# Optimization experiments

Hardware: AMD Instinct MI355X
Metric: run time of the kernel (lower is better)

Reference implementation:

```python
import jax, jax.numpy as jnp
import numpy as np

B, T, D, H = 2, 2048, 1024, 16  # batch, seq, hidden, heads; head_dim = 64


def setup_inputs() -> dict:
    key = jax.random.key(0)
    k1, k2, k3 = jax.random.split(key, 3)
    X = jax.random.normal(k1, (B, T, D), dtype=jnp.float32)
    # Dense(3*hidden_dim, use_bias=False): kernel [D, 3D]
    Wqkv = jax.random.normal(k2, (D, 3 * D), dtype=jnp.float32) / np.float32(np.sqrt(D))
    # Dense(hidden_dim, use_bias=False): kernel [D, D]
    Wproj = jax.random.normal(k3, (D, D), dtype=jnp.float32) / np.float32(np.sqrt(D))
    return {"X": X, "Wqkv": Wqkv, "Wproj": Wproj, "train": 0}


def reference(X, Wqkv, Wproj, train):
    # train=0 -> dropout is identity; the chunked online-softmax in the
    # original is mathematically exact softmax causal attention.
    b, t, d = X.shape
    hd = d // H
    qkv = X @ Wqkv                      # [B,T,3D]
    q, k, v = jnp.split(qkv, 3, axis=-1)
    q = q.reshape(b, t, H, hd)
    k = k.reshape(b, t, H, hd)
    v = v.reshape(b, t, H, hd)
    scale = 1.0 / jnp.sqrt(jnp.asarray(hd, dtype=X.dtype))
    scores = jnp.einsum('bqhd,bkhd->bhqk', q * scale, k)  # [B,H,T,T]
    causal = jnp.tril(jnp.ones((t, t), dtype=bool))
    scores = jnp.where(causal[None, None, :, :], scores, -jnp.inf)
    attn = jax.nn.softmax(scores, axis=-1)
    out = jnp.einsum('bhqk,bkhd->bqhd', attn, v).reshape(b, t, d)
    return out @ Wproj
```

## Files before the change

### kernel.cpp

```cpp
#include <hip/hip_runtime.h>


using u16 = unsigned short;
using u32 = unsigned int;

typedef __bf16 bf16x8 __attribute__((ext_vector_type(8)));
typedef __bf16 bf16x2 __attribute__((ext_vector_type(2)));
typedef float f32x4 __attribute__((ext_vector_type(4)));

#define DEV __device__ __forceinline__

DEV u16 f2bf(float f) { __bf16 h = (__bf16)f; return *(u16*)&h; }

DEV float bf2f(u16 v) {
  union { u32 u; float f; } x; x.u = (u32)v << 16; return x.f;
}

DEV u32 pk2(float lo, float hi) {
  bf16x2 t = {(__bf16)lo, (__bf16)hi};
  return *(u32*)&t;
}

DEV f32x4 mfma16(bf16x8 a, bf16x8 b, f32x4 c) {
  return __builtin_amdgcn_mfma_f32_16x16x32_bf16(a, b, c, 0, 0, 0);
}

DEV void gload_lds16(const void* g, void* l) {
  __builtin_amdgcn_global_load_lds(
      (const __attribute__((address_space(1))) void*)g,
      (__attribute__((address_space(3))) void*)l, 16, 0, 0);
}

DEV bf16x8 ld16(const u16* p) { return *(const bf16x8*)p; }

DEV void BAR() {
  __builtin_amdgcn_s_barrier();
  __builtin_amdgcn_sched_barrier(0);
}

DEV int vperm(int slot) {
  return ((((slot >> 4) & 2) | ((slot >> 2) & 1)) << 4) + (((slot >> 3) & 3) << 2) + (slot & 3);
}
DEV int vperm_inv(int k) {
  return (k & 0x23) | ((k & 0x10) >> 2) | ((k & 0x0c) << 1);
}


__global__ __launch_bounds__(256) void prep_kernel(
    const float* __restrict__ X, u16* __restrict__ Xb,
    const float* __restrict__ Wqkv, u16* __restrict__ Wqkvt,
    const float* __restrict__ Wproj, u16* __restrict__ Wprojt) {
  const int bid = blockIdx.x;
  const int t = threadIdx.x;

  if (bid < 2048) {
    int i = (bid * 256 + t) * 8;
    float4 a = *(const float4*)&X[i];
    float4 b = *(const float4*)&X[i + 4];
    union { u16 u[8]; uint4 v; } o;
    o.u[0] = f2bf(a.x); o.u[1] = f2bf(a.y); o.u[2] = f2bf(a.z); o.u[3] = f2bf(a.w);
    o.u[4] = f2bf(b.x); o.u[5] = f2bf(b.y); o.u[6] = f2bf(b.z); o.u[7] = f2bf(b.w);
    *(uint4*)&Xb[i] = o.v;
    return;
  }

  __shared__ float tile[64][65];
  const float* W; u16* Wt; int C, tb;
  if (bid < 2816) { W = Wqkv;  Wt = Wqkvt;  C = 3072; tb = bid - 2048; }
  else            { W = Wproj; Wt = Wprojt; C = 1024; tb = bid - 2816; }
  const int tilesC = C >> 6;
  const int tr = tb / tilesC, tc = tb % tilesC;
#pragma unroll
  for (int j = 0; j < 16; ++j) {
    int idx = j * 256 + t;
    int r = idx >> 6, c = idx & 63;
    tile[r][c] = W[(tr * 64 + r) * C + tc * 64 + c];
  }
  __syncthreads();
#pragma unroll
  for (int j = 0; j < 16; ++j) {
    int idx = j * 256 + t;
    int r = idx >> 6, c = idx & 63;
    Wt[(tc * 64 + r) * 1024 + tr * 64 + c] = f2bf(tile[c][r]);
  }
}


__global__ __launch_bounds__(512, 2) void gemm256_qkv_kernel(
    const u16* __restrict__ A, const u16* __restrict__ Bt,
    u16* __restrict__ Qb, u16* __restrict__ Kb, u16* __restrict__ VtP) {
  int bid = blockIdx.x;
  int bid2 = (bid & 7) * 24 + (bid >> 3);
  const int mt = bid2 / 12, nt = bid2 % 12;
  const int m0 = mt * 256, n0 = nt * 256;
  const int tid = threadIdx.x;
  const int wid = tid >> 6, lane = tid & 63;
  const int g = lane >> 4, li = lane & 15;
  const int wm = wid >> 2, wn = wid & 3;

  __shared__ __align__(16) u16 lds[65536];

  const int srow = lane >> 3;
  const int scol = ((lane & 7) * 8) ^ ((srow & 7) << 3);

  auto ISSUE = [&](int s, int kt) {
    const int p = kt & 1;
    const u16* base = (s < 2) ? &A[(size_t)(m0 + s * 128) * 1024]
                              : &Bt[(size_t)(n0 + (s - 2) * 128) * 1024];
#pragma unroll
    for (int is2 = 0; is2 < 2; ++is2) {
      int row = is2 * 64 + wid * 8 + srow;
      gload_lds16(&base[(size_t)row * 1024 + kt * 64 + scol],
                  &lds[s * 16384 + p * 8192 + is2 * 4096 + wid * 512]);
    }
  };

  auto LDA = [&](int p, int ks, bf16x8* aF) {
#pragma unroll
    for (int mi = 0; mi < 8; ++mi) {
      int row = mi * 16 + li;
      aF[mi] = ld16(&lds[wm * 16384 + p * 8192 + row * 64 +
                         ((ks * 32 + g * 8) ^ ((li & 7) << 3))]);
    }
  };
  auto LDB = [&](int p, int ks, bf16x8* bF) {
    int s = 2 + (wn >> 1);
#pragma unroll
    for (int ni = 0; ni < 4; ++ni) {
      int row = (wn & 1) * 64 + ni * 16 + li;
      bF[ni] = ld16(&lds[s * 16384 + p * 8192 + row * 64 +
                         ((ks * 32 + g * 8) ^ ((li & 7) << 3))]);
    }
  };

  f32x4 acc[8][4] = {};
  bf16x8 a0[8], a1[8], bF[4];

  ISSUE(0, 0); ISSUE(1, 0); ISSUE(2, 0); ISSUE(3, 0);
  ISSUE(0, 1); ISSUE(1, 1); ISSUE(2, 1);
  asm volatile("s_waitcnt vmcnt(6)" ::: "memory");
  BAR();

  for (int t = 0; t < 16; ++t) {
    const int p = t & 1;
    LDB(p, 0, bF);
    LDA(p, 0, a0);
    if (t + 1 < 16) ISSUE(3, t + 1);
    BAR();
    __builtin_amdgcn_s_setprio(1);
#pragma unroll
    for (int mi = 0; mi < 8; ++mi) {
      acc[mi][0] = mfma16(a0[mi], bF[0], acc[mi][0]);
      acc[mi][1] = mfma16(a0[mi], bF[1], acc[mi][1]);
    }
    __builtin_amdgcn_s_setprio(0);
    BAR();
    LDA(p, 1, a1);
    BAR();
    __builtin_amdgcn_s_setprio(1);
#pragma unroll
    for (int mi = 0; mi < 8; ++mi) {
      acc[mi][2] = mfma16(a0[mi], bF[2], acc[mi][2]);
      acc[mi][3] = mfma16(a0[mi], bF[3], acc[mi][3]);
    }
    __builtin_amdgcn_s_setprio(0);
    BAR();
    LDB(p, 1, bF);
    BAR();
    __builtin_amdgcn_s_setprio(1);
#pragma unroll
    for (int mi = 0; mi < 8; ++mi) {
      acc[mi][0] = mfma16(a1[mi], bF[0], acc[mi][0]);
      acc[mi][1] = mfma16(a1[mi], bF[1], acc[mi][1]);
    }
    __builtin_amdgcn_s_setprio(0);
    BAR();
    if (t + 2 < 16) { ISSUE(0, t + 2); ISSUE(1, t + 2); ISSUE(2, t + 2); }
    BAR();
    __builtin_amdgcn_s_setprio(1);
#pragma unroll
    for (int mi = 0; mi < 8; ++mi) {
      acc[mi][2] = mfma16(a1[mi], bF[2], acc[mi][2]);
      acc[mi][3] = mfma16(a1[mi], bF[3], acc[mi][3]);
    }
    __builtin_amdgcn_s_setprio(0);
    if (t + 2 < 16) {
      asm volatile("s_waitcnt vmcnt(6)" ::: "memory");
    } else {
      asm volatile("s_waitcnt vmcnt(0)" ::: "memory");
    }
    BAR();
  }

#pragma unroll
  for (int mi = 0; mi < 8; ++mi)
#pragma unroll
    for (int ni = 0; ni < 4; ++ni) {
      int cc = n0 + wn * 64 + ni * 16 + li;
      int which = cc >> 10, rem = cc & 1023;
      int h = rem >> 6, dd = rem & 63;
      int rbase = m0 + wm * 128 + mi * 16 + g * 4;
      int bb = rbase >> 11, tt = rbase & 2047;
      if (which == 2) {
        int slot0 = (tt & ~63) + vperm_inv(tt & 63);
        size_t di = ((size_t)(bb * 16 + h) * 64 + dd) * 2048 + slot0;
        uint2 wv;
        wv.x = pk2(acc[mi][ni][0], acc[mi][ni][1]);
        wv.y = pk2(acc[mi][ni][2], acc[mi][ni][3]);
        *(uint2*)&VtP[di] = wv;
      } else {
        u16* dst = which == 0 ? Qb : Kb;
        float sc = which == 0 ? 0.18033688f : 1.0f;
        size_t di = ((size_t)(bb * 16 + h) * 2048 + tt) * 64 + dd;
#pragma unroll
        for (int r = 0; r < 4; ++r) dst[di + (size_t)r * 64] = f2bf(acc[mi][ni][r] * sc);
      }
    }
}

__global__ __launch_bounds__(256) void gemm_proj_kernel(
    const u16* __restrict__ A, const u16* __restrict__ Bt, float* __restrict__ OF) {
  constexpr int NTN = 1024 / 128;
  const int mt = blockIdx.x / NTN, nt = blockIdx.x % NTN;
  const int m0 = mt * 128, n0 = nt * 128;
  const int tid = threadIdx.x;
  const int wid = tid >> 6, lane = tid & 63;
  const int g = lane >> 4, li = lane & 15;
  const int wm = wid >> 1, wn = wid & 1;

  __shared__ __align__(16) u16 As[2][128 * 64];
  __shared__ __align__(16) u16 Bs[2][128 * 64];

  f32x4 acc[4][4] = {};

  auto ISSUE = [&](int buf, int kt) {
#pragma unroll
    for (int iss = 0; iss < 4; ++iss) {
      int e = iss * 2048 + wid * 512 + lane * 8;
      int row = e >> 6;
      int kk = (e & 63) ^ ((row & 7) << 3);
      gload_lds16(&A[(size_t)(m0 + row) * 1024 + kt * 64 + kk], &As[buf][iss * 2048 + wid * 512]);
      gload_lds16(&Bt[(size_t)(n0 + row) * 1024 + kt * 64 + kk], &Bs[buf][iss * 2048 + wid * 512]);
    }
  };

  ISSUE(0, 0);
  __syncthreads();
  int cur = 0;

  for (int kt = 0; kt < 16; ++kt) {
    if (kt + 1 < 16) ISSUE(cur ^ 1, kt + 1);
#pragma unroll
    for (int ks = 0; ks < 2; ++ks) {
      bf16x8 af[4], bfr[4];
#pragma unroll
      for (int mi = 0; mi < 4; ++mi)
        af[mi] = ld16(&As[cur][(wm * 64 + mi * 16 + li) * 64 +
                               ((ks * 32 + g * 8) ^ ((li & 7) << 3))]);
#pragma unroll
      for (int ni = 0; ni < 4; ++ni)
        bfr[ni] = ld16(&Bs[cur][(wn * 64 + ni * 16 + li) * 64 +
                                ((ks * 32 + g * 8) ^ ((li & 7) << 3))]);
#pragma unroll
      for (int mi = 0; mi < 4; ++mi)
#pragma unroll
        for (int ni = 0; ni < 4; ++ni)
          acc[mi][ni] = mfma16(af[mi], bfr[ni], acc[mi][ni]);
    }
    __syncthreads();
    cur ^= 1;
  }

#pragma unroll
  for (int mi = 0; mi < 4; ++mi)
#pragma unroll
    for (int ni = 0; ni < 4; ++ni)
#pragma unroll
      for (int r = 0; r < 4; ++r) {
        int rr = m0 + wm * 64 + mi * 16 + g * 4 + r;
        int cc = n0 + wn * 64 + ni * 16 + li;
        OF[(size_t)rr * 1024 + cc] = acc[mi][ni][r];
      }
}


__global__ __launch_bounds__(256) void attn_kernel(const u16* __restrict__ Q,
                                                   const u16* __restrict__ K,
                                                   const u16* __restrict__ VtP,
                                                   u16* __restrict__ AO,
                                                   u16* __restrict__ P2O,
                                                   float* __restrict__ L1,
                                                   float* __restrict__ L2) {
  const int bid = blockIdx.x;
  const int idx = bid >> 5;
  const int qt = 31 - (idx >> 1);
  const int half = idx & 1;
  const int bh = bid & 31;
  const int b = bh >> 4, h = bh & 15;
  const int tid = threadIdx.x;
  const int wid = tid >> 6, lane = tid & 63;
  const int g = lane >> 4, li = lane & 15;
  const int q0 = qt * 64;
  const int kmid = (qt + 2) >> 1;
  const int k0 = half ? kmid : 0;
  const int k1 = half ? qt + 1 : kmid;

  if (k0 >= k1) {
    if (tid < 64) L2[(size_t)bh * 2048 + q0 + tid] = 0.f;
    return;
  }

  __shared__ __align__(16) u16 Ks[2][64 * 64];
  __shared__ __align__(16) u16 Vs[2][64 * 64];

  const u16* Qh = Q + (size_t)bh * 2048 * 64;
  const u16* Kh = K + (size_t)bh * 2048 * 64;
  const u16* Vh = VtP + (size_t)bh * 64 * 2048;

  const int qrow = q0 + wid * 16 + li;
  bf16x8 qf[2];
#pragma unroll
  for (int ks = 0; ks < 2; ++ks)
    qf[ks] = ld16(&Qh[(size_t)qrow * 64 + ks * 32 + g * 8]);

  f32x4 accO[4] = {};
  f32x4 accL = {};
  union { u32 u[4]; bf16x8 v; } ones;
  ones.u[0] = ones.u[1] = ones.u[2] = ones.u[3] = 0x3F803F80u;

  auto STAGE = [&](int buf, int ktile) {
#pragma unroll
    for (int iss = 0; iss < 2; ++iss) {
      int e = iss * 2048 + wid * 512 + lane * 8;
      int row = e >> 6;
      int c0 = (e & 63) ^ ((row & 7) << 3);
      gload_lds16(&Kh[(size_t)(ktile * 64 + row) * 64 + c0],
                  &Ks[buf][iss * 2048 + wid * 512]);
      gload_lds16(&Vh[(size_t)row * 2048 + ktile * 64 + c0],
                  &Vs[buf][iss * 2048 + wid * 512]);
    }
  };

  STAGE(0, k0);
  int cur = 0;

  for (int kt = k0; kt < k1; ++kt) {
    __syncthreads();
    if (kt + 1 < k1) STAGE(cur ^ 1, kt + 1);

    f32x4 s[4];
#pragma unroll
    for (int ni = 0; ni < 4; ++ni) s[ni] = f32x4{0.f, 0.f, 0.f, 0.f};
#pragma unroll
    for (int ks = 0; ks < 2; ++ks) {
      bf16x8 kf[4];
#pragma unroll
      for (int ni = 0; ni < 4; ++ni)
        kf[ni] = ld16(&Ks[cur][(ni * 16 + li) * 64 + ((ks * 32 + g * 8) ^ ((li & 7) << 3))]);
#pragma unroll
      for (int ni = 0; ni < 4; ++ni) s[ni] = mfma16(kf[ni], qf[ks], s[ni]);
    }

    if (kt == qt) {
      int ql = wid * 16 + li;
#pragma unroll
      for (int ni = 0; ni < 4; ++ni)
#pragma unroll
        for (int r = 0; r < 4; ++r)
          if (ni * 16 + g * 4 + r > ql) s[ni][r] = -1e30f;
    }

#pragma unroll
    for (int ni = 0; ni < 4; ++ni)
#pragma unroll
      for (int r = 0; r < 4; ++r) s[ni][r] = exp2f(s[ni][r]);

    union { u32 u[4]; bf16x8 v; } pf0, pf1;
    pf0.u[0] = pk2(s[0][0], s[0][1]); pf0.u[1] = pk2(s[0][2], s[0][3]);
    pf0.u[2] = pk2(s[1][0], s[1][1]); pf0.u[3] = pk2(s[1][2], s[1][3]);
    pf1.u[0] = pk2(s[2][0], s[2][1]); pf1.u[1] = pk2(s[2][2], s[2][3]);
    pf1.u[2] = pk2(s[3][0], s[3][1]); pf1.u[3] = pk2(s[3][2], s[3][3]);

    accL = mfma16(ones.v, pf0.v, accL);
    accL = mfma16(ones.v, pf1.v, accL);

#pragma unroll
    for (int ks = 0; ks < 2; ++ks) {
      bf16x8 pf = ks ? pf1.v : pf0.v;
#pragma unroll
      for (int mi = 0; mi < 4; ++mi) {
        bf16x8 vf = ld16(&Vs[cur][(mi * 16 + li) * 64 + ((ks * 32 + g * 8) ^ ((li & 7) << 3))]);
        accO[mi] = mfma16(vf, pf, accO[mi]);
      }
    }
    cur ^= 1;
  }

  if (g == 0) (half ? L2 : L1)[(size_t)bh * 2048 + qrow] = accL[0];
  __syncthreads();
  u16* E = (u16*)Ks;
  int erow = wid * 16 + li;
#pragma unroll
  for (int mi = 0; mi < 4; ++mi) {
    uint2 wv;
    wv.x = pk2(accO[mi][0], accO[mi][1]);
    wv.y = pk2(accO[mi][2], accO[mi][3]);
    *(uint2*)&E[erow * 64 + ((mi * 16 + g * 4) ^ ((li & 7) << 3))] = wv;
  }
  __syncthreads();
#pragma unroll
  for (int pass = 0; pass < 2; ++pass) {
    int idx2 = pass * 2048 + tid * 8;
    int row = idx2 >> 6, col = idx2 & 63;
    uint4 val = *(uint4*)&E[row * 64 + (col ^ ((row & 7) << 3))];
    if (half == 0)
      *(uint4*)&AO[(size_t)(b * 2048 + q0 + row) * 1024 + h * 64 + col] = val;
    else
      *(uint4*)&P2O[((size_t)bh * 2048 + q0 + row) * 64 + col] = val;
  }
}

__global__ __launch_bounds__(256) void combine_kernel(u16* __restrict__ AO,
                                                      const u16* __restrict__ P2O,
                                                      const float* __restrict__ L1,
                                                      const float* __restrict__ L2) {
  int gid = blockIdx.x * 256 + threadIdx.x;
  int row = gid >> 3, dp = (gid & 7) * 8;
  int bh = row >> 11, q = row & 2047;
  int b = bh >> 4, h = bh & 15;
  float l2 = L2[row];
  float inv = 1.0f / (L1[row] + l2);
  float w2 = (l2 == 0.f) ? 0.f : inv;
  u16* ao = &AO[(size_t)(b * 2048 + q) * 1024 + h * 64 + dp];
  const u16* p2 = &P2O[(size_t)row * 64 + dp];
  union { uint4 v; u16 u[8]; } o1, o2, w;
  o1.v = *(const uint4*)ao;
  o2.v = *(const uint4*)p2;
#pragma unroll
  for (int j = 0; j < 8; ++j)
    w.u[j] = f2bf(bf2f(o1.u[j]) * inv + bf2f(o2.u[j]) * w2);
  *(uint4*)ao = w.v;
}


extern "C" void kernel_launch(void* const* d_in, const int* in_sizes, int n_in,
                              void* d_out, int out_size, void* d_ws, size_t ws_size,
                              hipStream_t stream) {
  const float* X = (const float*)d_in[0];
  const float* Wqkv = (const float*)d_in[1];
  const float* Wproj = (const float*)d_in[2];
  float* out = (float*)d_out;

  u16* ws = (u16*)d_ws;
  u16* Xb = ws;
  u16* Wqkvt = Xb + 4194304;
  u16* Wprojt = Wqkvt + 3145728;
  u16* Qb = Wprojt + 1048576;
  u16* Kb = Qb + 4194304;
  u16* VtP = Kb + 4194304;
  u16* AO = VtP + 4194304;
  u16* P2O = Xb;
  float* L1 = (float*)Wqkvt;
  float* L2 = L1 + 65536;

  prep_kernel<<<3072, 256, 0, stream>>>(X, Xb, Wqkv, Wqkvt, Wproj, Wprojt);
  gemm256_qkv_kernel<<<192, 512, 0, stream>>>(Xb, Wqkvt, Qb, Kb, VtP);
  attn_kernel<<<2048, 256, 0, stream>>>(Qb, Kb, VtP, AO, P2O, L1, L2);
  combine_kernel<<<2048, 256, 0, stream>>>(AO, P2O, L1, L2);
  gemm_proj_kernel<<<32 * 8, 256, 0, stream>>>(AO, Wprojt, out);
}
```

Baseline: 110.0 us.

## Replace 256x256 QKV GEMM with simpler 128x128 double-buffered tile kernel

Swaps the hand-scheduled 256x256-tile QKV projection GEMM (512 threads, interleaved barriers and setprio) for a 128x128-tile kernel with 256 threads and a plain double-buffered global-to-LDS pipeline. The grid grows from 192 to 768 blocks, which spreads the work over more of the compute units and raises occupancy. The cost is lower operand reuse per tile, so more global and LDS traffic, and the loss of the finely interleaved MFMA/load scheduling.

```diff
diff --git a/kernel.cpp b/kernel.cpp
--- a/kernel.cpp
+++ b/kernel.cpp
@@ -32,11 +32,6 @@
 }
 
 DEV bf16x8 ld16(const u16* p) { return *(const bf16x8*)p; }
-
-DEV void BAR() {
-  __builtin_amdgcn_s_barrier();
-  __builtin_amdgcn_sched_barrier(0);
-}
 
 DEV int vperm(int slot) {
   return ((((slot >> 4) & 2) | ((slot >> 2) & 1)) << 4) + (((slot >> 3) & 3) << 2) + (slot & 3);
@@ -86,120 +81,70 @@
 }
 
 
-__global__ __launch_bounds__(512, 2) void gemm256_qkv_kernel(
+__global__ __launch_bounds__(256, 4) void gemm_qkv_kernel(
     const u16* __restrict__ A, const u16* __restrict__ Bt,
     u16* __restrict__ Qb, u16* __restrict__ Kb, u16* __restrict__ VtP) {
   int bid = blockIdx.x;
-  int bid2 = (bid & 7) * 24 + (bid >> 3);
-  const int mt = bid2 / 12, nt = bid2 % 12;
-  const int m0 = mt * 256, n0 = nt * 256;
+  int bid2 = (bid & 7) * 96 + (bid >> 3);
+  constexpr int NTN = 3072 / 128;
+  const int mt = bid2 / NTN, nt = bid2 % NTN;
+  const int m0 = mt * 128, n0 = nt * 128;
   const int tid = threadIdx.x;
   const int wid = tid >> 6, lane = tid & 63;
   const int g = lane >> 4, li = lane & 15;
-  const int wm = wid >> 2, wn = wid & 3;
-
-  __shared__ __align__(16) u16 lds[65536];
-
-  const int srow = lane >> 3;
-  const int scol = ((lane & 7) * 8) ^ ((srow & 7) << 3);
-
-  auto ISSUE = [&](int s, int kt) {
-    const int p = kt & 1;
-    const u16* base = (s < 2) ? &A[(size_t)(m0 + s * 128) * 1024]
-                              : &Bt[(size_t)(n0 + (s - 2) * 128) * 1024];
-#pragma unroll
-    for (int is2 = 0; is2 < 2; ++is2) {
-      int row = is2 * 64 + wid * 8 + srow;
-      gload_lds16(&base[(size_t)row * 1024 + kt * 64 + scol],
-                  &lds[s * 16384 + p * 8192 + is2 * 4096 + wid * 512]);
+  const int wm = wid >> 1, wn = wid & 1;
+
+  __shared__ __align__(16) u16 As[2][128 * 64];
+  __shared__ __align__(16) u16 Bs[2][128 * 64];
+
+  f32x4 acc[4][4] = {};
+
+  auto ISSUE = [&](int buf, int kt) {
+#pragma unroll
+    for (int iss = 0; iss < 4; ++iss) {
+      int e = iss * 2048 + wid * 512 + lane * 8;
+      int row = e >> 6;
+      int kk = (e & 63) ^ ((row & 7) << 3);
+      gload_lds16(&A[(size_t)(m0 + row) * 1024 + kt * 64 + kk], &As[buf][iss * 2048 + wid * 512]);
+      gload_lds16(&Bt[(size_t)(n0 + row) * 1024 + kt * 64 + kk], &Bs[buf][iss * 2048 + wid * 512]);
     }
   };
 
-  auto LDA = [&](int p, int ks, bf16x8* aF) {
-#pragma unroll
-    for (int mi = 0; mi < 8; ++mi) {
-      int row = mi * 16 + li;
-      aF[mi] = ld16(&lds[wm * 16384 + p * 8192 + row * 64 +
-                         ((ks * 32 + g * 8) ^ ((li & 7) << 3))]);
-    }
-  };
-  auto LDB = [&](int p, int ks, bf16x8* bF) {
-    int s = 2 + (wn >> 1);
-#pragma unroll
-    for (int ni = 0; ni < 4; ++ni) {
-      int row = (wn & 1) * 64 + ni * 16 + li;
-      bF[ni] = ld16(&lds[s * 16384 + p * 8192 + row * 64 +
-                         ((ks * 32 + g * 8) ^ ((li & 7) << 3))]);
-    }
-  };
-
-  f32x4 acc[8][4] = {};
-  bf16x8 a0[8], a1[8], bF[4];
-
-  ISSUE(0, 0); ISSUE(1, 0); ISSUE(2, 0); ISSUE(3, 0);
-  ISSUE(0, 1); ISSUE(1, 1); ISSUE(2, 1);
-  asm volatile("s_waitcnt vmcnt(6)" ::: "memory");
-  BAR();
-
-  for (int t = 0; t < 16; ++t) {
-    const int p = t & 1;
-    LDB(p, 0, bF);
-    LDA(p, 0, a0);
-    if (t + 1 < 16) ISSUE(3, t + 1);
-    BAR();
-    __builtin_amdgcn_s_setprio(1);
-#pragma unroll
-    for (int mi = 0; mi < 8; ++mi) {
-      acc[mi][0] = mfma16(a0[mi], bF[0], acc[mi][0]);
-      acc[mi][1] = mfma16(a0[mi], bF[1], acc[mi][1]);
-    }
-    __builtin_amdgcn_s_setprio(0);
-    BAR();
-    LDA(p, 1, a1);
-    BAR();
-    __builtin_amdgcn_s_setprio(1);
-#pragma unroll
-    for (int mi = 0; mi < 8; ++mi) {
-      acc[mi][2] = mfma16(a0[mi], bF[2], acc[mi][2]);
-      acc[mi][3] = mfma16(a0[mi], bF[3], acc[mi][3]);
-    }
-    __builtin_amdgcn_s_setprio(0);
-    BAR();
-    LDB(p, 1, bF);
-    BAR();
-    __builtin_amdgcn_s_setprio(1);
-#pragma unroll
-    for (int mi = 0; mi < 8; ++mi) {
-      acc[mi][0] = mfma16(a1[mi], bF[0], acc[mi][0]);
-      acc[mi][1] = mfma16(a1[mi], bF[1], acc[mi][1]);
-    }
-    __builtin_amdgcn_s_setprio(0);
-    BAR();
-    if (t + 2 < 16) { ISSUE(0, t + 2); ISSUE(1, t + 2); ISSUE(2, t + 2); }
-    BAR();
-    __builtin_amdgcn_s_setprio(1);
-#pragma unroll
-    for (int mi = 0; mi < 8; ++mi) {
-      acc[mi][2] = mfma16(a1[mi], bF[2], acc[mi][2]);
-      acc[mi][3] = mfma16(a1[mi], bF[3], acc[mi][3]);
-    }
-    __builtin_amdgcn_s_setprio(0);
-    if (t + 2 < 16) {
-      asm volatile("s_waitcnt vmcnt(6)" ::: "memory");
-    } else {
-      asm volatile("s_waitcnt vmcnt(0)" ::: "memory");
-    }
-    BAR();
-  }
-
-#pragma unroll
-  for (int mi = 0; mi < 8; ++mi)
+  ISSUE(0, 0);
+  __syncthreads();
+  int cur = 0;
+
+  for (int kt = 0; kt < 16; ++kt) {
+    if (kt + 1 < 16) ISSUE(cur ^ 1, kt + 1);
+#pragma unroll
+    for (int ks = 0; ks < 2; ++ks) {
+      bf16x8 af[4], bfr[4];
+#pragma unroll
+      for (int mi = 0; mi < 4; ++mi)
+        af[mi] = ld16(&As[cur][(wm * 64 + mi * 16 + li) * 64 +
+                               ((ks * 32 + g * 8) ^ ((li & 7) << 3))]);
+#pragma unroll
+      for (int ni = 0; ni < 4; ++ni)
+        bfr[ni] = ld16(&Bs[cur][(wn * 64 + ni * 16 + li) * 64 +
+                                ((ks * 32 + g * 8) ^ ((li & 7) << 3))]);
+#pragma unroll
+      for (int mi = 0; mi < 4; ++mi)
+#pragma unroll
+        for (int ni = 0; ni < 4; ++ni)
+          acc[mi][ni] = mfma16(af[mi], bfr[ni], acc[mi][ni]);
+    }
+    __syncthreads();
+    cur ^= 1;
+  }
+
+#pragma unroll
+  for (int mi = 0; mi < 4; ++mi)
 #pragma unroll
     for (int ni = 0; ni < 4; ++ni) {
       int cc = n0 + wn * 64 + ni * 16 + li;
       int which = cc >> 10, rem = cc & 1023;
       int h = rem >> 6, dd = rem & 63;
-      int rbase = m0 + wm * 128 + mi * 16 + g * 4;
+      int rbase = m0 + wm * 64 + mi * 16 + g * 4;
       int bb = rbase >> 11, tt = rbase & 2047;
       if (which == 2) {
         int slot0 = (tt & ~63) + vperm_inv(tt & 63);
@@ -464,7 +409,7 @@
   float* L2 = L1 + 65536;
 
   prep_kernel<<<3072, 256, 0, stream>>>(X, Xb, Wqkv, Wqkvt, Wproj, Wprojt);
-  gemm256_qkv_kernel<<<192, 512, 0, stream>>>(Xb, Wqkvt, Qb, Kb, VtP);
+  gemm_qkv_kernel<<<768, 256, 0, stream>>>(Xb, Wqkvt, Qb, Kb, VtP);
   attn_kernel<<<2048, 256, 0, stream>>>(Qb, Kb, VtP, AO, P2O, L1, L2);
   combine_kernel<<<2048, 256, 0, stream>>>(AO, P2O, L1, L2);
   gemm_proj_kernel<<<32 * 8, 256, 0, stream>>>(AO, Wprojt, out);
```

After: 125.4 us. 1.14x slower.
